# Kernel tuning notes

Measured on AMD Instinct MI355X. Metric: run time of the kernel, lower is better.

## Reference

```python
import jax, jax.numpy as jnp
import numpy as np
import math


def _bilinear_sample(fea, gx, gy):
    # fea: (C, Hs, Ws); gx, gy: (P,) pixel coords. zeros padding, align_corners=True.
    C, Hs, Ws = fea.shape
    x0 = jnp.floor(gx)
    y0 = jnp.floor(gy)
    wx = gx - x0
    wy = gy - y0

    def tap(xi, yi):
        valid = (xi >= 0) & (xi <= Ws - 1) & (yi >= 0) & (yi <= Hs - 1)
        xc = jnp.clip(xi, 0, Ws - 1).astype(jnp.int32)
        yc = jnp.clip(yi, 0, Hs - 1).astype(jnp.int32)
        return fea[:, yc, xc] * valid.astype(fea.dtype)  # (C, P)

    return (tap(x0, y0) * (1 - wx) * (1 - wy)
            + tap(x0 + 1, y0) * wx * (1 - wy)
            + tap(x0, y0 + 1) * (1 - wx) * wy
            + tap(x0 + 1, y0 + 1) * wx * wy)


def homo_warping(src_fea, src_proj, ref_proj, depth_values):
    # src_fea: (B,C,Hs,Ws); projs: (B,4,4); depth_values: (B,D,Hr,Wr)
    B, C, Hs, Ws = src_fea.shape
    _, D, Hr, Wr = depth_values.shape
    proj = src_proj @ jnp.linalg.inv(ref_proj)
    rot = proj[:, :3, :3]
    trans = proj[:, :3, 3:4]
    yy, xx = jnp.meshgrid(jnp.arange(Hr, dtype=src_fea.dtype),
                          jnp.arange(Wr, dtype=src_fea.dtype), indexing='ij')
    xyz = jnp.stack([xx.ravel(), yy.ravel(), jnp.ones(Hr * Wr, src_fea.dtype)])  # (3, HW)
    rot_xyz = jnp.einsum('bij,jp->bip', rot, xyz)  # (B,3,HW)
    pts = rot_xyz[:, :, None, :] * depth_values.reshape(B, 1, D, Hr * Wr) + trans[:, :, :, None]
    z = pts[:, 2]
    z = jnp.where(z == 0, 1e-9, z)
    # grid is computed under torch.no_grad() in the original -> stop_gradient
    gx = jax.lax.stop_gradient((pts[:, 0] / z).reshape(B, D * Hr * Wr))
    gy = jax.lax.stop_gradient((pts[:, 1] / z).reshape(B, D * Hr * Wr))
    warped = jax.vmap(_bilinear_sample)(src_fea, gx, gy)  # (B, C, D*Hr*Wr)
    return warped.reshape(B, C, D, Hr, Wr)


def setup_inputs() -> dict:
    key = jax.random.key(0)
    B, C, H, W, D, N = 2, 32, 128, 160, 32, 4
    k1, k2, k3 = jax.random.split(key, 3)
    ref_feature = jax.random.normal(k1, (B, C, H, W), jnp.float32)
    src_features = jax.random.normal(k2, (N, B, C, H, W), jnp.float32)
    # proj_matrices: (B, nviews, 2, 4, 4); [...,0]=extrinsic 4x4, [...,1]=intrinsic 4x4
    K = np.eye(4, dtype=np.float32)
    K[0, 0] = 300.0; K[1, 1] = 300.0; K[0, 2] = W / 2.0; K[1, 2] = H / 2.0
    projs = np.zeros((B, N + 1, 2, 4, 4), np.float32)
    for v in range(N + 1):
        a = 0.03 * v
        Rm = np.array([[np.cos(a), 0.0, np.sin(a)],
                       [0.0, 1.0, 0.0],
                       [-np.sin(a), 0.0, np.cos(a)]], np.float32)
        E = np.eye(4, dtype=np.float32)
        E[:3, :3] = Rm
        E[:3, 3] = np.array([20.0 * v, 5.0 * v, 0.0], np.float32)
        projs[:, v, 0] = E
        projs[:, v, 1] = K
    proj_matrices = jnp.asarray(projs)
    depth_hypo = jnp.broadcast_to(
        jnp.linspace(425.0, 935.0, D, dtype=jnp.float32)[None, :, None, None], (B, D, H, W))
    reg_w = jax.random.normal(k3, (8,), jnp.float32)
    reg_b = jnp.zeros((1,), jnp.float32)
    return {"ref_feature": ref_feature, "src_features": src_features,
            "proj_matrices": proj_matrices, "depth_hypo": depth_hypo,
            "reg_w": reg_w, "reg_b": reg_b}


def reference(ref_feature, src_features, proj_matrices, depth_hypo, reg_w, reg_b):
    attn_temp = 2.0
    G = 8  # group_cor_dim; group_cor=True path
    B, D, H, W = depth_hypo.shape
    C = ref_feature.shape[1]
    ref_proj = proj_matrices[:, 0]
    ref_proj_new = ref_proj[:, 0].at[:, :3, :4].set(
        jnp.einsum('bij,bjk->bik', ref_proj[:, 1, :3, :3], ref_proj[:, 0, :3, :4]))
    # ref_volume broadcast over D via size-1 depth axis (B,G,C/G,1,H,W)
    ref_g = ref_feature.reshape(B, G, C // G, 1, H, W)
    cor_weight_sum = 1e-8
    cor_feats = 0.0
    n_src = src_features.shape[0]
    for src_idx in range(n_src):  # fixed small number of source views
        src_proj = proj_matrices[:, src_idx + 1]
        src_proj_new = src_proj[:, 0].at[:, :3, :4].set(
            jnp.einsum('bij,bjk->bik', src_proj[:, 1, :3, :3], src_proj[:, 0, :3, :4]))
        warped = homo_warping(src_features[src_idx], src_proj_new, ref_proj_new, depth_hypo)
        cor_feat = (warped.reshape(B, G, C // G, D, H, W) * ref_g).mean(2)  # (B,G,D,H,W)
        cor_weight = jax.nn.softmax(cor_feat.sum(1) / attn_temp, axis=1) / math.sqrt(C)  # (B,D,H,W)
        cor_weight_sum = cor_weight_sum + cor_weight
        cor_feats = cor_feats + cor_weight[:, None] * cor_feat
    cor_feats = cor_feats / cor_weight_sum[:, None]
    # regnet stand-in: 1x1x1 conv over the G group channels -> (B,D,H,W) logits
    attn_logits = jnp.einsum('bgdhw,g->bdhw', cor_feats, reg_w) + reg_b[0]
    attn_weight = jax.nn.softmax(attn_logits, axis=1)
    idx = jnp.argmax(attn_weight, axis=1, keepdims=True)
    depth = jnp.take_along_axis(depth_hypo, idx, axis=1).squeeze(1)  # (B,H,W)
    return depth, attn_weight
```

## Files before the change

### kernel.cpp

```cpp
#include <hip/hip_runtime.h>
#include <hip/hip_bf16.h>
#include <math.h>

#define BB 2
#define CC 32
#define HH 128
#define WW 160
#define DD 32
#define NN 4
#define HW (HH * WW)
#define GG 8

__device__ void compute_mats(int t, const float* __restrict__ proj,
                             float* __restrict__ mats) {
    int b = t >> 2, n = t & 3;
    const float* Er = proj + ((size_t)(b * (NN + 1) + 0) * 2 + 0) * 16;
    const float* Kr = proj + ((size_t)(b * (NN + 1) + 0) * 2 + 1) * 16;
    const float* Es = proj + ((size_t)(b * (NN + 1) + n + 1) * 2 + 0) * 16;
    const float* Ks = proj + ((size_t)(b * (NN + 1) + n + 1) * 2 + 1) * 16;

    double A[4][4], Bm[4][4];
    for (int r = 0; r < 4; r++)
        for (int c = 0; c < 4; c++) {
            if (r < 3) {
                A[r][c]  = (double)Kr[r*4+0]*Er[0*4+c] + (double)Kr[r*4+1]*Er[1*4+c] + (double)Kr[r*4+2]*Er[2*4+c];
                Bm[r][c] = (double)Ks[r*4+0]*Es[0*4+c] + (double)Ks[r*4+1]*Es[1*4+c] + (double)Ks[r*4+2]*Es[2*4+c];
            } else {
                A[r][c]  = (double)Er[12 + c];
                Bm[r][c] = (double)Es[12 + c];
            }
        }
    double M[4][8];
    for (int i = 0; i < 4; i++)
        for (int j = 0; j < 4; j++) { M[i][j] = A[i][j]; M[i][4+j] = (i == j) ? 1.0 : 0.0; }
    for (int col = 0; col < 4; col++) {
        int piv = col;
        for (int r = col + 1; r < 4; r++)
            if (fabs(M[r][col]) > fabs(M[piv][col])) piv = r;
        if (piv != col)
            for (int j = 0; j < 8; j++) { double tmp = M[col][j]; M[col][j] = M[piv][j]; M[piv][j] = tmp; }
        double pv = M[col][col];
        for (int j = 0; j < 8; j++) M[col][j] /= pv;
        for (int r = 0; r < 4; r++) {
            if (r == col) continue;
            double f = M[r][col];
            for (int j = 0; j < 8; j++) M[r][j] -= f * M[col][j];
        }
    }
    float* o = mats + t * 12;
    for (int i = 0; i < 3; i++) {
        double p0 = 0, p1 = 0, p2 = 0, p3 = 0;
        for (int k = 0; k < 4; k++) {
            p0 += Bm[i][k] * M[k][4+0];
            p1 += Bm[i][k] * M[k][4+1];
            p2 += Bm[i][k] * M[k][4+2];
            p3 += Bm[i][k] * M[k][4+3];
        }
        o[i*3+0] = (float)p0; o[i*3+1] = (float)p1; o[i*3+2] = (float)p2;
        o[9 + i] = (float)p3;
    }
}

__global__ __launch_bounds__(256) void prep_transpose(const float* __restrict__ src,
                                                      const float* __restrict__ ref,
                                                      const float* __restrict__ proj,
                                                      float* __restrict__ srcT,
                                                      float* __restrict__ refT,
                                                      float* __restrict__ mats) {
    if (blockIdx.x == 0 && blockIdx.y == 0 && threadIdx.x < 8)
        compute_mats(threadIdx.x, proj, mats);

    __shared__ float t[32][33];
    int slab = blockIdx.y;
    const float* ip;
    float* op;
    if (slab < 8) { ip = src + (size_t)slab * 32 * HW; op = srcT + (size_t)slab * 32 * HW; }
    else          { ip = ref + (size_t)(slab - 8) * 32 * HW; op = refT + (size_t)(slab - 8) * 32 * HW; }
    int hw0 = blockIdx.x * 32;
    int tx = threadIdx.x & 31, ty = threadIdx.x >> 5;
#pragma unroll
    for (int i = 0; i < 4; i++) {
        int c = ty + i * 8;
        t[c][tx] = ip[(size_t)c * HW + hw0 + tx];
    }
    __syncthreads();
#pragma unroll
    for (int i = 0; i < 4; i++) {
        int hl = ty + i * 8;
        op[(size_t)(hw0 + hl) * 32 + tx] = t[tx][hl];
    }
}

__global__ __launch_bounds__(256) void main_kernel(
    const float* __restrict__ srcT,
    const float* __restrict__ refT,
    const float* __restrict__ depth,
    const float* __restrict__ mats,
    const float* __restrict__ regw,
    const float* __restrict__ regb,
    float* __restrict__ out)
{
    int tid = threadIdx.x;
    int g  = tid & 7;
    int d  = tid >> 3;

    int p   = blockIdx.x;
    int b   = p / HW;
    int rem = p - b * HW;
    int y   = rem / WW;
    int x   = rem - y * WW;
    float fx = (float)x, fy = (float)y;

    float4 R = *(const float4*)(refT + (size_t)p * 32 + g * 4);
    float dep = depth[((size_t)(b * DD + d) * HH + y) * WW + x];
    float rwg = regw[g];
    float rb  = regb[0];

    __shared__ float sL[NN][DD];
    __shared__ float sCW[NN][DD];
    __shared__ float sCWS[DD];
    __shared__ float sE[DD];
    __shared__ float sDep[DD];

    if (g == 0) sDep[d] = dep;

    float W00, W10, W01, W11;
    int   I00, I10, I01, I11;
    {
        int n0 = tid & 3;
        const float* Mp = mats + (size_t)(b * NN + n0) * 12;
        float ax = Mp[0] * fx + Mp[1] * fy + Mp[2];
        float ay = Mp[3] * fx + Mp[4] * fy + Mp[5];
        float az = Mp[6] * fx + Mp[7] * fy + Mp[8];
        float px = ax * dep + Mp[9];
        float py = ay * dep + Mp[10];
        float pz = az * dep + Mp[11];
        float z  = (pz == 0.f) ? 1e-9f : pz;
        float gx = px / z, gy = py / z;

        float x0f = floorf(gx), y0f = floorf(gy);
        float wx = gx - x0f, wy = gy - y0f;
        bool vx0 = (x0f >= 0.f)  && (x0f <= (float)(WW - 1));
        bool vx1 = (x0f >= -1.f) && (x0f <= (float)(WW - 2));
        bool vy0 = (y0f >= 0.f)  && (y0f <= (float)(HH - 1));
        bool vy1 = (y0f >= -1.f) && (y0f <= (float)(HH - 2));
        W00 = (vx0 && vy0) ? (1.f - wx) * (1.f - wy) : 0.f;
        W10 = (vx1 && vy0) ? wx * (1.f - wy)         : 0.f;
        W01 = (vx0 && vy1) ? (1.f - wx) * wy         : 0.f;
        W11 = (vx1 && vy1) ? wx * wy                 : 0.f;

        int xi0 = (int)fminf(fmaxf(x0f,       0.f), (float)(WW - 1));
        int xi1 = (int)fminf(fmaxf(x0f + 1.f, 0.f), (float)(WW - 1));
        int yi0 = (int)fminf(fmaxf(y0f,       0.f), (float)(HH - 1));
        int yi1 = (int)fminf(fmaxf(y0f + 1.f, 0.f), (float)(HH - 1));
        I00 = yi0 * WW + xi0;
        I10 = yi0 * WW + xi1;
        I01 = yi1 * WW + xi0;
        I11 = yi1 * WW + xi1;
    }

    float cor[NN];

#pragma unroll
    for (int n = 0; n < NN; n++) {
        int src_lane = (tid & 56) | n;
        float w00 = __shfl(W00, src_lane);
        float w10 = __shfl(W10, src_lane);
        float w01 = __shfl(W01, src_lane);
        float w11 = __shfl(W11, src_lane);
        int   i00 = __shfl(I00, src_lane);
        int   i10 = __shfl(I10, src_lane);
        int   i01 = __shfl(I01, src_lane);
        int   i11 = __shfl(I11, src_lane);

        const float4* S4 = (const float4*)(srcT + (size_t)(n * BB + b) * (32 * HW));
        float4 a  = S4[(size_t)i00 * 8 + g];
        float4 bq = S4[(size_t)i10 * 8 + g];
        float4 c  = S4[(size_t)i01 * 8 + g];
        float4 e  = S4[(size_t)i11 * 8 + g];

        float wrx = w00 * a.x + w10 * bq.x + w01 * c.x + w11 * e.x;
        float wry = w00 * a.y + w10 * bq.y + w01 * c.y + w11 * e.y;
        float wrz = w00 * a.z + w10 * bq.z + w01 * c.z + w11 * e.z;
        float wrw = w00 * a.w + w10 * bq.w + w01 * c.w + w11 * e.w;
        float cr = wrx * R.x + wry * R.y + wrz * R.z + wrw * R.w;
        cor[n] = cr;

        float ls = cr;
        ls += __shfl_xor(ls, 1);
        ls += __shfl_xor(ls, 2);
        ls += __shfl_xor(ls, 4);
        if (g == 0) sL[n][d] = ls * 0.125f;
    }
    __syncthreads();

    if (tid < 64) {
        int n  = tid >> 4;
        int dh = tid & 15;
        float l0 = sL[n][dh];
        float l1 = sL[n][dh + 16];
        float m = fmaxf(l0, l1);
        m = fmaxf(m, __shfl_xor(m, 1));
        m = fmaxf(m, __shfl_xor(m, 2));
        m = fmaxf(m, __shfl_xor(m, 4));
        m = fmaxf(m, __shfl_xor(m, 8));
        float e0 = __expf(l0 - m), e1 = __expf(l1 - m);
        float s = e0 + e1;
        s += __shfl_xor(s, 1);
        s += __shfl_xor(s, 2);
        s += __shfl_xor(s, 4);
        s += __shfl_xor(s, 8);
        float f = 0.17677669529663687f / s;
        float c0 = e0 * f, c1 = e1 * f;
        sCW[n][dh]      = c0;
        sCW[n][dh + 16] = c1;
        float t0 = c0, t1 = c1;
        t0 += __shfl_xor(t0, 16); t0 += __shfl_xor(t0, 32);
        t1 += __shfl_xor(t1, 16); t1 += __shfl_xor(t1, 32);
        if (n == 0) {
            sCWS[dh]      = t0 + 1e-8f;
            sCWS[dh + 16] = t1 + 1e-8f;
        }
    }
    __syncthreads();

    float cf = 0.f;
#pragma unroll
    for (int n = 0; n < NN; n++) cf += sCW[n][d] * cor[n];
    cf *= 0.25f;
    float v = cf * rwg;
    v += __shfl_xor(v, 1);
    v += __shfl_xor(v, 2);
    v += __shfl_xor(v, 4);
    float logit2 = v / sCWS[d] + rb;
    if (g == 0) sE[d] = logit2;
    __syncthreads();

    if (tid < 64) {
        int dl = tid & 31;
        float q = sE[dl];
        float m2 = q;
        m2 = fmaxf(m2, __shfl_xor(m2, 1));
        m2 = fmaxf(m2, __shfl_xor(m2, 2));
        m2 = fmaxf(m2, __shfl_xor(m2, 4));
        m2 = fmaxf(m2, __shfl_xor(m2, 8));
        m2 = fmaxf(m2, __shfl_xor(m2, 16));
        float e2 = __expf(q - m2);
        float t2 = e2;
        t2 += __shfl_xor(t2, 1);
        t2 += __shfl_xor(t2, 2);
        t2 += __shfl_xor(t2, 4);
        t2 += __shfl_xor(t2, 8);
        t2 += __shfl_xor(t2, 16);
        float aw = e2 / t2;
        if (tid < 32)
            out[(size_t)BB * HW + (size_t)(b * DD + dl) * HW + rem] = aw;

        float bv = q; int bi = dl;
#pragma unroll
        for (int s = 1; s <= 16; s <<= 1) {
            float ov = __shfl_xor(bv, s);
            int   oi = __shfl_xor(bi, s);
            if (ov > bv || (ov == bv && oi < bi)) { bv = ov; bi = oi; }
        }
        if (tid < 32 && dl == bi) out[p] = sDep[bi];
    }
}

extern "C" void kernel_launch(void* const* d_in, const int* in_sizes, int n_in,
                              void* d_out, int out_size, void* d_ws, size_t ws_size,
                              hipStream_t stream) {
    const float* ref   = (const float*)d_in[0];
    const float* src   = (const float*)d_in[1];
    const float* proj  = (const float*)d_in[2];
    const float* depth = (const float*)d_in[3];
    const float* regw  = (const float*)d_in[4];
    const float* regb  = (const float*)d_in[5];
    float* out = (float*)d_out;

    float* ws   = (float*)d_ws;
    float* mats = ws;
    float* srcT = ws + 256;
    float* refT = srcT + (size_t)NN * BB * HW * 32;

    prep_transpose<<<dim3(HW / 32, 10), 256, 0, stream>>>(src, ref, proj,
                                                          srcT, refT, mats);
    main_kernel<<<BB * HW, 256, 0, stream>>>(srcT, refT, depth, mats,
                                             regw, regb, out);
}
```

Baseline: 200.1 us.

## Double-buffer gather loads, stage matrices in LDS, use packed math and rcp

Restructures the per-view gather loop so the four bilinear taps for two views are in flight before they are consumed, overlapping memory latency with arithmetic. The projection matrices are staged in shared memory and read as float4. Divisions become hardware reciprocals, the dot products use packed 2-wide float vectors, and launch bounds now request 6 waves per SIMD. The extra in-flight registers could lower occupancy or cause spills, and the approximate reciprocal can move floor boundaries and change argmax results slightly.

```diff
diff --git a/kernel.cpp b/kernel.cpp
--- a/kernel.cpp
+++ b/kernel.cpp
@@ -10,6 +10,8 @@
 #define NN 4
 #define HW (HH * WW)
 #define GG 8
+
+typedef float v2f __attribute__((ext_vector_type(2)));
 
 __device__ void compute_mats(int t, const float* __restrict__ proj,
                              float* __restrict__ mats) {
@@ -91,7 +93,7 @@
     }
 }
 
-__global__ __launch_bounds__(256) void main_kernel(
+__global__ __launch_bounds__(256, 6) void main_kernel(
     const float* __restrict__ srcT,
     const float* __restrict__ refT,
     const float* __restrict__ depth,
@@ -111,32 +113,39 @@
     int x   = rem - y * WW;
     float fx = (float)x, fy = (float)y;
 
-    float4 R = *(const float4*)(refT + (size_t)p * 32 + g * 4);
-    float dep = depth[((size_t)(b * DD + d) * HH + y) * WW + x];
-    float rwg = regw[g];
-    float rb  = regb[0];
-
+    __shared__ float sM[48];
     __shared__ float sL[NN][DD];
     __shared__ float sCW[NN][DD];
     __shared__ float sCWS[DD];
     __shared__ float sE[DD];
     __shared__ float sDep[DD];
 
+    if (tid < 48) sM[tid] = mats[(size_t)b * 48 + tid];
+
+    float4 R = *(const float4*)(refT + (size_t)p * 32 + g * 4);
+    v2f Rlo = { R.x, R.y }, Rhi = { R.z, R.w };
+    float dep = depth[((size_t)(b * DD + d) * HH + y) * WW + x];
+    float rwg = regw[g];
+    float rb  = regb[0];
     if (g == 0) sDep[d] = dep;
+    __syncthreads();
 
     float W00, W10, W01, W11;
     int   I00, I10, I01, I11;
     {
         int n0 = tid & 3;
-        const float* Mp = mats + (size_t)(b * NN + n0) * 12;
-        float ax = Mp[0] * fx + Mp[1] * fy + Mp[2];
-        float ay = Mp[3] * fx + Mp[4] * fy + Mp[5];
-        float az = Mp[6] * fx + Mp[7] * fy + Mp[8];
-        float px = ax * dep + Mp[9];
-        float py = ay * dep + Mp[10];
-        float pz = az * dep + Mp[11];
+        float4 m0 = *(const float4*)(sM + n0 * 12);
+        float4 m1 = *(const float4*)(sM + n0 * 12 + 4);
+        float4 m2 = *(const float4*)(sM + n0 * 12 + 8);
+        float ax = m0.x * fx + m0.y * fy + m0.z;
+        float ay = m0.w * fx + m1.x * fy + m1.y;
+        float az = m1.z * fx + m1.w * fy + m2.x;
+        float px = ax * dep + m2.y;
+        float py = ay * dep + m2.z;
+        float pz = az * dep + m2.w;
         float z  = (pz == 0.f) ? 1e-9f : pz;
-        float gx = px / z, gy = py / z;
+        float rz = __builtin_amdgcn_rcpf(z);
+        float gx = px * rz, gy = py * rz;
 
         float x0f = floorf(gx), y0f = floorf(gy);
         float wx = gx - x0f, wy = gy - y0f;
@@ -159,39 +168,54 @@
         I11 = yi1 * WW + xi1;
     }
 
-    float cor[NN];
-
+    float4 Wn[NN];
+    int4   In[NN];
 #pragma unroll
     for (int n = 0; n < NN; n++) {
         int src_lane = (tid & 56) | n;
-        float w00 = __shfl(W00, src_lane);
-        float w10 = __shfl(W10, src_lane);
-        float w01 = __shfl(W01, src_lane);
-        float w11 = __shfl(W11, src_lane);
-        int   i00 = __shfl(I00, src_lane);
-        int   i10 = __shfl(I10, src_lane);
-        int   i01 = __shfl(I01, src_lane);
-        int   i11 = __shfl(I11, src_lane);
-
+        Wn[n].x = __shfl(W00, src_lane);
+        Wn[n].y = __shfl(W10, src_lane);
+        Wn[n].z = __shfl(W01, src_lane);
+        Wn[n].w = __shfl(W11, src_lane);
+        In[n].x = __shfl(I00, src_lane);
+        In[n].y = __shfl(I10, src_lane);
+        In[n].z = __shfl(I01, src_lane);
+        In[n].w = __shfl(I11, src_lane);
+    }
+
+    float cor[NN];
+    float4 ta[2], tb[2], tc[2], te[2];
+
+    auto issue = [&](int n, int s) {
         const float4* S4 = (const float4*)(srcT + (size_t)(n * BB + b) * (32 * HW));
-        float4 a  = S4[(size_t)i00 * 8 + g];
-        float4 bq = S4[(size_t)i10 * 8 + g];
-        float4 c  = S4[(size_t)i01 * 8 + g];
-        float4 e  = S4[(size_t)i11 * 8 + g];
-
-        float wrx = w00 * a.x + w10 * bq.x + w01 * c.x + w11 * e.x;
-        float wry = w00 * a.y + w10 * bq.y + w01 * c.y + w11 * e.y;
-        float wrz = w00 * a.z + w10 * bq.z + w01 * c.z + w11 * e.z;
-        float wrw = w00 * a.w + w10 * bq.w + w01 * c.w + w11 * e.w;
-        float cr = wrx * R.x + wry * R.y + wrz * R.z + wrw * R.w;
+        ta[s] = S4[(size_t)In[n].x * 8 + g];
+        tb[s] = S4[(size_t)In[n].y * 8 + g];
+        tc[s] = S4[(size_t)In[n].z * 8 + g];
+        te[s] = S4[(size_t)In[n].w * 8 + g];
+    };
+    auto consume = [&](int n, int s) {
+        float4 a = ta[s], bq = tb[s], c = tc[s], e = te[s];
+        v2f alo = { a.x, a.y },  ahi = { a.z, a.w };
+        v2f blo = { bq.x, bq.y }, bhi = { bq.z, bq.w };
+        v2f clo = { c.x, c.y },  chi = { c.z, c.w };
+        v2f elo = { e.x, e.y },  ehi = { e.z, e.w };
+        float w00 = Wn[n].x, w10 = Wn[n].y, w01 = Wn[n].z, w11 = Wn[n].w;
+        v2f wlo = w00 * alo + w10 * blo + w01 * clo + w11 * elo;
+        v2f whi = w00 * ahi + w10 * bhi + w01 * chi + w11 * ehi;
+        v2f pr  = wlo * Rlo + whi * Rhi;
+        float cr = pr.x + pr.y;
         cor[n] = cr;
-
         float ls = cr;
         ls += __shfl_xor(ls, 1);
         ls += __shfl_xor(ls, 2);
         ls += __shfl_xor(ls, 4);
         if (g == 0) sL[n][d] = ls * 0.125f;
-    }
+    };
+
+    issue(0, 0); issue(1, 1);
+    consume(0, 0); issue(2, 0);
+    consume(1, 1); issue(3, 1);
+    consume(2, 0); consume(3, 1);
     __syncthreads();
 
     if (tid < 64) {
@@ -232,7 +256,7 @@
     v += __shfl_xor(v, 1);
     v += __shfl_xor(v, 2);
     v += __shfl_xor(v, 4);
-    float logit2 = v / sCWS[d] + rb;
+    float logit2 = v * __builtin_amdgcn_rcpf(sCWS[d]) + rb;
     if (g == 0) sE[d] = logit2;
     __syncthreads();
 
```

Measured after the change: 206.8 us. +3.4%, slower.
